# Performance work log

Hardware: AMD Instinct MI355X
Metric: run time of the kernel (lower is better)

Reference implementation:

```python
import jax, jax.numpy as jnp
import numpy as np

# Dimensions (match init_kwargs / input_specs)
NF, NLOC, NALL = 1, 1024, 2048
N_DIM, E_DIM, A_DIM = 128, 16, 64
NNEI, A_SEL, AXIS = 120, 20, 4

act = jax.nn.silu


def _lin(key, i, o):
    k1, k2 = jax.random.split(key)
    w = jax.random.normal(k1, (i, o), jnp.float32) / np.float32(np.sqrt(i))
    b = jax.random.normal(k2, (o,), jnp.float32) * 0.01
    return w, b


def setup_inputs() -> dict:
    key = jax.random.key(0)
    ks = jax.random.split(key, 16)
    d = {}
    d["node_ebd_ext"] = jax.random.normal(ks[0], (NF, NALL, N_DIM), jnp.float32)
    d["edge_ebd"] = jax.random.normal(ks[1], (NF, NLOC, NNEI, E_DIM), jnp.float32)
    d["h2"] = jax.random.normal(ks[2], (NF, NLOC, NNEI, 3), jnp.float32)
    d["angle_ebd"] = jax.random.normal(ks[3], (NF, NLOC, A_SEL, A_SEL, A_DIM), jnp.float32)
    d["sw"] = jax.random.uniform(ks[4], (NF, NLOC, NNEI), jnp.float32)
    d["a_sw"] = jax.random.uniform(ks[5], (NF, NLOC, A_SEL), jnp.float32)
    d["nlist"] = jax.random.randint(ks[6], (NF, NLOC, NNEI), 0, NALL)
    d["nlist_mask"] = jnp.ones((NF, NLOC, NNEI), bool)
    d["a_nlist_mask"] = jnp.ones((NF, NLOC, A_SEL), bool)
    edge_info_dim = 2 * N_DIM + E_DIM          # 272
    angle_dim = A_DIM + N_DIM + 2 * E_DIM      # 224 (a_compress_rate == 0)
    d["w_node_self"], d["b_node_self"] = _lin(ks[7], N_DIM, N_DIM)
    d["w_node_sym"], d["b_node_sym"] = _lin(ks[8], (N_DIM + E_DIM) * AXIS, N_DIM)
    d["w_node_edge"], d["b_node_edge"] = _lin(ks[9], edge_info_dim, N_DIM)
    d["w_edge_self"], d["b_edge_self"] = _lin(ks[10], edge_info_dim, E_DIM)
    d["w_ea1"], d["b_ea1"] = _lin(ks[11], angle_dim, E_DIM)
    d["w_ea2"], d["b_ea2"] = _lin(ks[12], E_DIM, E_DIM)
    d["w_angle_self"], d["b_angle_self"] = _lin(ks[13], angle_dim, A_DIM)
    # res_residual update style: one learnable residual scale per update branch,
    # init 'const' with update_residual = 0.1
    d["n_res"] = jnp.full((3, N_DIM), 0.1, jnp.float32)  # self, sym, edge-message
    d["e_res"] = jnp.full((2, E_DIM), 0.1, jnp.float32)  # self, angle-message
    d["a_res"] = jnp.full((1, A_DIM), 0.1, jnp.float32)  # self
    return d


def _forward(node_ebd_ext, edge_ebd, h2, angle_ebd, sw, a_sw,
             w_node_self, b_node_self, w_node_sym, b_node_sym,
             w_node_edge, b_node_edge, w_edge_self, b_edge_self,
             w_ea1, b_ea1, w_ea2, b_ea2, w_angle_self, b_angle_self,
             n_res, e_res, a_res, nlist, nlist_mask, a_nlist_mask):
    nf, nall, n_dim = node_ebd_ext.shape
    _, nloc, nnei, e_dim = edge_ebd.shape
    a_sel = angle_ebd.shape[2]
    node_ebd = node_ebd_ext[:, :nloc]

    # gather neighbor node embeddings: nf x nloc x nnei x n_dim
    nei_node = jax.vmap(lambda tbl, idx: tbl[idx])(node_ebd_ext, nlist)
    nei_node = jnp.where(nlist_mask[..., None], nei_node, 0.0)

    # 1) node self update
    node_self_update = act(node_ebd @ w_node_self + b_node_self)

    # 2) node symmetrization update (grrg over both edge and neighbor-node features)
    wgt = (sw * nlist_mask)[..., None]

    def sym(ebd):
        e = ebd * wgt
        hg = jnp.einsum('flni,flnd->flid', h2, e) / np.float32(nnei)  # f,l,3,d
        grrg = jnp.einsum('flid,flia->flda', hg, hg[..., :AXIS]) / np.float32(3.0)
        return grrg.reshape(nf, nloc, -1)

    node_sym_in = jnp.concatenate([sym(nei_node), sym(edge_ebd)], axis=-1)
    node_sym_update = act(node_sym_in @ w_node_sym + b_node_sym)

    # 3) edge info = [node_i, node_j, edge_ij]
    node_i = jnp.broadcast_to(node_ebd[:, :, None, :], (nf, nloc, nnei, n_dim))
    edge_info = jnp.concatenate([node_i, nei_node, edge_ebd], axis=-1)

    # 3a) node <- edge message (sw-weighted mean over neighbors)
    node_edge_update = act(edge_info @ w_node_edge + b_node_edge) * sw[..., None]
    node_edge_update = node_edge_update.sum(axis=-2) / np.float32(nnei)

    node_new = (node_ebd + n_res[0] * node_self_update
                + n_res[1] * node_sym_update + n_res[2] * node_edge_update)

    # 4) edge self update
    edge_self_update = act(edge_info @ w_edge_self + b_edge_self)

    # 5) angle branch (a_compress_rate == 0)
    edge_for_angle = jnp.where(a_nlist_mask[..., None], edge_ebd[:, :, :a_sel, :], 0.0)
    node_angle = jnp.broadcast_to(node_ebd[:, :, None, None, :], (nf, nloc, a_sel, a_sel, n_dim))
    e_ik = jnp.broadcast_to(edge_for_angle[:, :, :, None, :], (nf, nloc, a_sel, a_sel, e_dim))
    e_ij = jnp.broadcast_to(edge_for_angle[:, :, None, :, :], (nf, nloc, a_sel, a_sel, e_dim))
    angle_info = jnp.concatenate([angle_ebd, node_angle, e_ik, e_ij], axis=-1)

    # edge <- angle message: sw-weighted reduce over one angle axis
    ea = act(angle_info @ w_ea1 + b_ea1)  # nf,nloc,a_sel,a_sel,e_dim
    weighted = a_sw[:, :, :, None, None] * a_sw[:, :, None, :, None] * ea
    reduced = weighted.sum(axis=-2) / np.float32(np.sqrt(a_sel))  # nf,nloc,a_sel,e_dim
    pad = jnp.zeros((nf, nloc, nnei - a_sel, e_dim), edge_ebd.dtype)
    padded = jnp.concatenate([reduced, pad], axis=2)
    full_mask = jnp.concatenate(
        [a_nlist_mask, jnp.zeros((nf, nloc, nnei - a_sel), bool)], axis=-1)
    # smooth_edge_update = False: keep original edge ebd where angle mask is off
    padded = jnp.where(full_mask[..., None], padded, edge_ebd)
    edge_angle_update = act(padded @ w_ea2 + b_ea2)

    edge_new = edge_ebd + e_res[0] * edge_self_update + e_res[1] * edge_angle_update

    # angle self update
    angle_self_update = act(angle_info @ w_angle_self + b_angle_self)
    angle_new = angle_ebd + a_res[0] * angle_self_update

    return node_new, edge_new, angle_new


def reference(node_ebd_ext, edge_ebd, h2, angle_ebd, sw, a_sw, nlist, nlist_mask,
              a_nlist_mask, w_node_self, b_node_self, w_node_sym, b_node_sym,
              w_node_edge, b_node_edge, w_edge_self, b_edge_self, w_ea1, b_ea1,
              w_ea2, b_ea2, w_angle_self, b_angle_self, n_res, e_res, a_res):
    return _forward(node_ebd_ext, edge_ebd, h2, angle_ebd, sw, a_sw,
                    w_node_self, b_node_self, w_node_sym, b_node_sym,
                    w_node_edge, b_node_edge, w_edge_self, b_edge_self,
                    w_ea1, b_ea1, w_ea2, b_ea2, w_angle_self, b_angle_self,
                    n_res, e_res, a_res, nlist, nlist_mask, a_nlist_mask)
```

## Files before the change

### kernel.cpp

```cpp
#include <hip/hip_runtime.h>
#include <math.h>

#define NLOC 1024
#define NALL 2048
#define NDIM 128
#define EDIM 16
#define ADIM 64
#define NNEI 120
#define ASEL 20


__device__ __forceinline__ float silu(float x) {
    return x * __builtin_amdgcn_rcpf(1.f + __expf(-x));
}

__device__ __forceinline__ unsigned short f2bf(float f) {
    unsigned int u = __float_as_uint(f);
    u += 0x7fffu + ((u >> 16) & 1u);
    return (unsigned short)(u >> 16);
}

typedef __attribute__((ext_vector_type(8))) short bf16x8;
typedef __attribute__((ext_vector_type(4))) float f32x4;

__global__ __launch_bounds__(256) void k_prep(
    const float* __restrict__ node_ext,
    const float* __restrict__ w_ne, const float* __restrict__ b_ne,
    const float* __restrict__ w_es, const float* __restrict__ b_es,
    const float* __restrict__ w_ea1, const float* __restrict__ b_ea1,
    const float* __restrict__ w_as, const float* __restrict__ b_as,
    float* __restrict__ proj, float* __restrict__ pre_e,
    float* __restrict__ pre_a, unsigned short* __restrict__ wtb)
{
    const int b = blockIdx.x, t = threadIdx.x;
    if (b == 3072) {
        for (int idx = t; idx < 64 * 80; idx += 256) {
            int k = idx / 80, o = idx - k * 80;
            float v = (o < 16) ? w_ea1[k * 16 + o] : w_as[k * 64 + (o - 16)];
            wtb[o * 64 + k] = f2bf(v);
        }
        return;
    }
    __shared__ float x[128];
    const int row = (b < 2048) ? b : (b - 2048);
    if (t < 128) x[t] = node_ext[row * 128 + t];
    __syncthreads();
    if (b < 2048) {
        if (t < 144) {
            float acc = 0.f;
            if (t < 128) {
                for (int k = 0; k < 128; k++) acc += x[k] * w_ne[(128 + k) * 128 + t];
            } else {
                int o = t - 128;
                for (int k = 0; k < 128; k++) acc += x[k] * w_es[(128 + k) * 16 + o];
            }
            proj[b * 144 + t] = acc;
        }
    } else {
        int i = b - 2048;
        if (t < 144) {
            float acc;
            if (t < 128) {
                acc = b_ne[t];
                for (int k = 0; k < 128; k++) acc += x[k] * w_ne[k * 128 + t];
            } else {
                int o = t - 128;
                acc = b_es[o];
                for (int k = 0; k < 128; k++) acc += x[k] * w_es[k * 16 + o];
            }
            pre_e[i * 144 + t] = acc;
        } else if (t < 224) {
            int o = t - 144;
            float acc;
            if (o < 16) {
                acc = b_ea1[o];
                for (int k = 0; k < 128; k++) acc += x[k] * w_ea1[(64 + k) * 16 + o];
            } else {
                int o2 = o - 16;
                acc = b_as[o2];
                for (int k = 0; k < 128; k++) acc += x[k] * w_as[(64 + k) * 64 + o2];
            }
            pre_a[i * 80 + o] = acc;
        }
    }
}

__global__ __launch_bounds__(256, 4) void k_angle(
    const float* __restrict__ angle, const float* __restrict__ edge,
    const float* __restrict__ asw,
    const float* __restrict__ w_ea1, const float* __restrict__ w_as,
    const unsigned short* __restrict__ wtb, const float* __restrict__ pre_a,
    const float* __restrict__ a_res,
    float* __restrict__ out_angle, float* __restrict__ reduced)
{
    const int i = blockIdx.x, t = threadIdx.x;
    const int lane = t & 63, wv = t >> 6;
    const int m = lane & 15, q = lane >> 4;

    __shared__ float eca_s[ASEL * 80], ecb_s[ASEL * 80], edge20_s[ASEL * EDIM];
    __shared__ float asw_s[ASEL], ares_s[ADIM], red_s[ASEL * 16];

    bf16x8 bfrag[5][2];
    #pragma unroll
    for (int nt = 0; nt < 5; nt++)
        #pragma unroll
        for (int ks = 0; ks < 2; ks++)
            bfrag[nt][ks] = *(const bf16x8*)&wtb[(nt * 16 + m) * 64 + ks * 32 + q * 8];

    for (int idx = t; idx < ASEL * EDIM; idx += 256)
        edge20_s[idx] = edge[(size_t)i * NNEI * EDIM + idx];
    if (t < ASEL) asw_s[t] = asw[i * ASEL + t];
    if (t < ADIM) ares_s[t] = a_res[t];
    for (int idx = t; idx < ASEL * 16; idx += 256) red_s[idx] = 0.f;
    __syncthreads();

    int mt = wv;
    float4 c0, c1, c2, c3;
    {
        const float* Arow = angle + ((size_t)i * 400 + mt * 16 + m) * 64 + q * 8;
        c0 = *(const float4*)(Arow + 0);
        c1 = *(const float4*)(Arow + 4);
        c2 = *(const float4*)(Arow + 32);
        c3 = *(const float4*)(Arow + 36);
    }

    for (int idx = t; idx < 2 * ASEL * 80; idx += 256) {
        int half = idx / 1600, rem = idx - half * 1600;
        int aa = rem / 80, o = rem - aa * 80;
        float acc = (half == 0) ? pre_a[i * 80 + o] : 0.f;
        if (o < 16) {
            const float* w = w_ea1 + (192 + half * 16) * 16 + o;
            #pragma unroll
            for (int k = 0; k < 16; k++) acc += edge20_s[aa * 16 + k] * w[k * 16];
        } else {
            const float* w = w_as + (192 + half * 16) * 64 + (o - 16);
            #pragma unroll
            for (int k = 0; k < 16; k++) acc += edge20_s[aa * 16 + k] * w[k * 64];
        }
        if (half == 0) eca_s[rem] = acc; else ecb_s[rem] = acc;
    }
    __syncthreads();

    for (; mt < 25; mt += 4) {
        const int nmt = mt + 4;
        float4 n0{}, n1{}, n2{}, n3{};
        if (nmt < 25) {
            const float* Arow = angle + ((size_t)i * 400 + nmt * 16 + m) * 64 + q * 8;
            n0 = *(const float4*)(Arow + 0);
            n1 = *(const float4*)(Arow + 4);
            n2 = *(const float4*)(Arow + 32);
            n3 = *(const float4*)(Arow + 36);
        }

        bf16x8 af0, af1;
        af0[0] = (short)f2bf(c0.x); af0[1] = (short)f2bf(c0.y);
        af0[2] = (short)f2bf(c0.z); af0[3] = (short)f2bf(c0.w);
        af0[4] = (short)f2bf(c1.x); af0[5] = (short)f2bf(c1.y);
        af0[6] = (short)f2bf(c1.z); af0[7] = (short)f2bf(c1.w);
        af1[0] = (short)f2bf(c2.x); af1[1] = (short)f2bf(c2.y);
        af1[2] = (short)f2bf(c2.z); af1[3] = (short)f2bf(c2.w);
        af1[4] = (short)f2bf(c3.x); af1[5] = (short)f2bf(c3.y);
        af1[6] = (short)f2bf(c3.z); af1[7] = (short)f2bf(c3.w);

        const int p0 = mt * 16 + q * 4;
        float rez[4][4];
        #pragma unroll
        for (int r = 0; r < 4; r++) {
            const float* ar = angle + ((size_t)i * 400 + p0 + r) * 64 + m - 16;
            #pragma unroll
            for (int nt = 1; nt < 5; nt++) rez[r][nt - 1] = ar[nt * 16];
        }

        f32x4 acc[5];
        #pragma unroll
        for (int nt = 0; nt < 5; nt++) {
            acc[nt] = (f32x4){0.f, 0.f, 0.f, 0.f};
            acc[nt] = __builtin_amdgcn_mfma_f32_16x16x32_bf16(af0, bfrag[nt][0], acc[nt], 0, 0, 0);
            acc[nt] = __builtin_amdgcn_mfma_f32_16x16x32_bf16(af1, bfrag[nt][1], acc[nt], 0, 0, 0);
        }

        #pragma unroll
        for (int r = 0; r < 4; r++) {
            const int p = p0 + r;
            const int a = p / 20;
            const int bb = p - a * 20;
            {
                const float s = acc[0][r] + eca_s[a * 80 + m] + ecb_s[bb * 80 + m];
                atomicAdd(&red_s[a * 16 + m], asw_s[bb] * silu(s));
            }
            const size_t base = ((size_t)i * 400 + p) * 64;
            #pragma unroll
            for (int nt = 1; nt < 5; nt++) {
                const int o = nt * 16 + m;
                const float s = acc[nt][r] + eca_s[a * 80 + o] + ecb_s[bb * 80 + o];
                out_angle[base + o - 16] = rez[r][nt - 1] + ares_s[o - 16] * silu(s);
            }
        }

        c0 = n0; c1 = n1; c2 = n2; c3 = n3;
    }
    __syncthreads();

    for (int idx = t; idx < ASEL * 16; idx += 256) {
        const int aa = idx >> 4;
        reduced[i * 320 + idx] = red_s[idx] * asw_s[aa] * 0.22360679774997896f;
    }
}

__global__ __launch_bounds__(256) void k_en(
    const float* __restrict__ edge, const float* __restrict__ h2,
    const float* __restrict__ sw, const int* __restrict__ nlist,
    const float* __restrict__ node_ext,
    const float* __restrict__ w_ne, const float* __restrict__ w_es,
    const float* __restrict__ w_ea2, const float* __restrict__ b_ea2,
    const float* __restrict__ e_res,
    const float* __restrict__ proj, const float* __restrict__ pre_e,
    const float* __restrict__ reduced,
    const float* __restrict__ w_ns, const float* __restrict__ b_ns,
    const float* __restrict__ w_sym, const float* __restrict__ b_sym,
    const float* __restrict__ n_res,
    float* __restrict__ out_edge, float* __restrict__ out_node)
{
    const int i = blockIdx.x, t = threadIdx.x;
    __shared__ float red_s[320], esu_s[120 * 17], pre_e_s[144];
    __shared__ float wea2_s[256], bea2_s[16], eres_s[32], sw_s[120];
    __shared__ float wes_s[256];
    __shared__ float edge_s[120 * 17];
    __shared__ float neu_part[2][128], neu_s[128];
    __shared__ int nl_s[120];
    __shared__ float node_s[128], hjc_s[120 * 4], hgN_s[3 * 128], hgE_s[3 * 16], sym_s[576];
    __shared__ float hgN_part[2][3][128];
    __shared__ float hgE_part[8][3][16];
    __shared__ float s2_part[128];

    for (int idx = t; idx < 320; idx += 256) red_s[idx] = reduced[i * 320 + idx];
    for (int idx = t; idx < 1920; idx += 256) {
        const int j = idx >> 4, k = idx & 15;
        edge_s[j * 17 + k] = edge[(size_t)i * 1920 + idx];
    }
    if (t < 144) pre_e_s[t] = pre_e[i * 144 + t];
    if (t < 128) node_s[t] = node_ext[i * 128 + t];
    if (t < 120) {
        nl_s[t] = nlist[i * 120 + t];
        const float s = sw[i * 120 + t];
        sw_s[t] = s;
        hjc_s[t * 4 + 0] = h2[((size_t)i * 120 + t) * 3 + 0] * s;
        hjc_s[t * 4 + 1] = h2[((size_t)i * 120 + t) * 3 + 1] * s;
        hjc_s[t * 4 + 2] = h2[((size_t)i * 120 + t) * 3 + 2] * s;
        hjc_s[t * 4 + 3] = 0.f;
    }
    if (t < 256) wea2_s[t] = w_ea2[t];
    if (t < 16) bea2_s[t] = b_ea2[t];
    if (t < 32) eres_s[t] = e_res[t];
    for (int idx = t; idx < 256; idx += 256) wes_s[idx] = w_es[256 * 16 + idx];
    __syncthreads();

    {
        const int o = t & 127, half = t >> 7;
        const int j0 = half * 60, j1 = j0 + 60;
        float w3c[16];
        #pragma unroll
        for (int k = 0; k < 16; k++) w3c[k] = w_ne[(256 + k) * 128 + o];
        const float pe = pre_e_s[o];
        float pj = proj[(size_t)nl_s[j0] * 144 + o];
        float acc = 0.f;
        for (int j = j0; j < j1; j++) {
            float pn = 0.f;
            if (j + 1 < j1) pn = proj[(size_t)nl_s[j + 1] * 144 + o];
            const float* er = &edge_s[j * 17];
            float s = pe + pj;
            #pragma unroll
            for (int k = 0; k < 16; k++) s += er[k] * w3c[k];
            acc += silu(s) * sw_s[j];
            pj = pn;
        }
        neu_part[half][o] = acc;
    }

    for (int idx = t; idx < 1920; idx += 256) {
        const int j = idx >> 4, oo = idx & 15;
        const int n = nl_s[j];
        float s = pre_e_s[128 + oo] + proj[(size_t)n * 144 + 128 + oo];
        #pragma unroll
        for (int k = 0; k < 16; k++) s += edge_s[j * 17 + k] * wes_s[k * 16 + oo];
        esu_s[j * 17 + oo] = silu(s);
    }
    __syncthreads();

    if (t < 128) neu_s[t] = (neu_part[0][t] + neu_part[1][t]) * (1.f / 120.f);

    {
        const int d = t & 127, half = t >> 7;
        const int j0 = half * 60, j1 = j0 + 60;
        float a0 = 0.f, a1 = 0.f, a2 = 0.f;
        float v = node_ext[(size_t)nl_s[j0] * 128 + d];
        for (int j = j0; j < j1; j++) {
            float vn = 0.f;
            if (j + 1 < j1) vn = node_ext[(size_t)nl_s[j + 1] * 128 + d];
            const float4 hc = *(const float4*)&hjc_s[j * 4];
            a0 += hc.x * v; a1 += hc.y * v; a2 += hc.z * v;
            v = vn;
        }
        hgN_part[half][0][d] = a0;
        hgN_part[half][1][d] = a1;
        hgN_part[half][2][d] = a2;
    }

    if (t < 128) {
        const int d = t & 15, ch = t >> 4;
        const int j0 = ch * 15;
        float a0 = 0.f, a1 = 0.f, a2 = 0.f;
        for (int j = j0; j < j0 + 15; j++) {
            const float v = edge_s[j * 17 + d];
            const float4 hc = *(const float4*)&hjc_s[j * 4];
            a0 += hc.x * v; a1 += hc.y * v; a2 += hc.z * v;
        }
        hgE_part[ch][0][d] = a0;
        hgE_part[ch][1][d] = a1;
        hgE_part[ch][2][d] = a2;
    }

    for (int idx = t; idx < 1920; idx += 256) {
        const int j = idx >> 4, o = idx & 15;
        float s = bea2_s[o];
        if (j < 20) {
            #pragma unroll
            for (int k = 0; k < 16; k++) s += red_s[j * 16 + k] * wea2_s[k * 16 + o];
        } else {
            const float* er = &edge_s[j * 17];
            #pragma unroll
            for (int k = 0; k < 16; k++) s += er[k] * wea2_s[k * 16 + o];
        }
        const float eau = silu(s);
        const float ev = edge_s[j * 17 + o];
        out_edge[((size_t)i * 120 + j) * 16 + o] =
            ev + eres_s[o] * esu_s[j * 17 + o] + eres_s[16 + o] * eau;
    }
    __syncthreads();

    if (t < 128) {
        hgN_s[0 * 128 + t] = (hgN_part[0][0][t] + hgN_part[1][0][t]) * (1.f / 120.f);
        hgN_s[1 * 128 + t] = (hgN_part[0][1][t] + hgN_part[1][1][t]) * (1.f / 120.f);
        hgN_s[2 * 128 + t] = (hgN_part[0][2][t] + hgN_part[1][2][t]) * (1.f / 120.f);
    } else if (t < 176) {
        const int c = (t - 128) >> 4, d = (t - 128) & 15;
        float s = 0.f;
        #pragma unroll
        for (int ch = 0; ch < 8; ch++) s += hgE_part[ch][c][d];
        hgE_s[c * 16 + d] = s * (1.f / 120.f);
    }
    __syncthreads();

    for (int idx = t; idx < 576; idx += 256) {
        if (idx < 512) {
            const int d = idx >> 2, a = idx & 3;
            sym_s[idx] = (hgN_s[d] * hgN_s[a] + hgN_s[128 + d] * hgN_s[128 + a] +
                          hgN_s[256 + d] * hgN_s[256 + a]) * (1.f / 3.f);
        } else {
            const int r = idx - 512, d = r >> 2, a = r & 3;
            sym_s[idx] = (hgE_s[d] * hgE_s[a] + hgE_s[16 + d] * hgE_s[16 + a] +
                          hgE_s[32 + d] * hgE_s[32 + a]) * (1.f / 3.f);
        }
    }
    __syncthreads();

    float s1 = 0.f, s2 = 0.f;
    {
        const int o = t & 127, half = t >> 7;
        if (half == 0) {
            s1 = b_ns[o];
            for (int k = 0; k < 128; k++) s1 += node_s[k] * w_ns[k * 128 + o];
            s2 = b_sym[o];
            for (int k = 0; k < 224; k++) s2 += sym_s[k] * w_sym[k * 128 + o];
        } else {
            for (int k = 224; k < 576; k++) s2 += sym_s[k] * w_sym[k * 128 + o];
            s2_part[o] = s2;
        }
    }
    __syncthreads();

    if (t < 128) {
        const float nsu = silu(s1);
        const float nsy = silu(s2 + s2_part[t]);
        out_node[i * 128 + t] = node_s[t] + n_res[t] * nsu + n_res[128 + t] * nsy +
                                n_res[256 + t] * neu_s[t];
    }
}

extern "C" void kernel_launch(void* const* d_in, const int* in_sizes, int n_in,
                              void* d_out, int out_size, void* d_ws, size_t ws_size,
                              hipStream_t stream)
{
    const float* node_ext = (const float*)d_in[0];
    const float* edge     = (const float*)d_in[1];
    const float* h2       = (const float*)d_in[2];
    const float* angle    = (const float*)d_in[3];
    const float* sw       = (const float*)d_in[4];
    const float* asw      = (const float*)d_in[5];
    const int*   nlist    = (const int*)d_in[6];
    const float* w_ns  = (const float*)d_in[9];  const float* b_ns  = (const float*)d_in[10];
    const float* w_sym = (const float*)d_in[11]; const float* b_sym = (const float*)d_in[12];
    const float* w_ne  = (const float*)d_in[13]; const float* b_ne  = (const float*)d_in[14];
    const float* w_es  = (const float*)d_in[15]; const float* b_es  = (const float*)d_in[16];
    const float* w_ea1 = (const float*)d_in[17]; const float* b_ea1 = (const float*)d_in[18];
    const float* w_ea2 = (const float*)d_in[19]; const float* b_ea2 = (const float*)d_in[20];
    const float* w_as  = (const float*)d_in[21]; const float* b_as  = (const float*)d_in[22];
    const float* n_res = (const float*)d_in[23];
    const float* e_res = (const float*)d_in[24];
    const float* a_res = (const float*)d_in[25];

    float* out_node  = (float*)d_out;
    float* out_edge  = out_node + (size_t)NLOC * NDIM;
    float* out_angle = out_edge + (size_t)NLOC * NNEI * EDIM;

    float* ws      = (float*)d_ws;
    float* proj    = ws;
    float* pre_e   = proj + 2048 * 144;
    float* pre_a   = pre_e + 1024 * 144;
    float* reduced = pre_a + 1024 * 80;
    unsigned short* wtb = (unsigned short*)(reduced + 1024 * 320);

    k_prep<<<dim3(3073), dim3(256), 0, stream>>>(node_ext, w_ne, b_ne, w_es, b_es,
                                                 w_ea1, b_ea1, w_as, b_as,
                                                 proj, pre_e, pre_a, wtb);
    k_angle<<<dim3(1024), dim3(256), 0, stream>>>(angle, edge, asw, w_ea1, w_as,
                                                  wtb, pre_a, a_res, out_angle, reduced);
    k_en<<<dim3(1024), dim3(256), 0, stream>>>(edge, h2, sw, nlist, node_ext,
                                               w_ne, w_es, w_ea2, b_ea2, e_res,
                                               proj, pre_e, reduced,
                                               w_ns, b_ns, w_sym, b_sym, n_res,
                                               out_edge, out_node);
}
```

Baseline: 351.9 us.

## Fuse angle and edge/node kernels into one per-atom kernel with shared-memory union

```diff
diff --git a/kernel.cpp b/kernel.cpp
--- a/kernel.cpp
+++ b/kernel.cpp
@@ -85,20 +85,52 @@
     }
 }
 
-__global__ __launch_bounds__(256, 4) void k_angle(
+__global__ __launch_bounds__(256, 4) void k_fused(
     const float* __restrict__ angle, const float* __restrict__ edge,
     const float* __restrict__ asw,
     const float* __restrict__ w_ea1, const float* __restrict__ w_as,
     const unsigned short* __restrict__ wtb, const float* __restrict__ pre_a,
     const float* __restrict__ a_res,
-    float* __restrict__ out_angle, float* __restrict__ reduced)
+    const float* __restrict__ h2, const float* __restrict__ sw,
+    const int* __restrict__ nlist, const float* __restrict__ node_ext,
+    const float* __restrict__ w_ne, const float* __restrict__ w_es,
+    const float* __restrict__ w_ea2, const float* __restrict__ b_ea2,
+    const float* __restrict__ e_res,
+    const float* __restrict__ proj, const float* __restrict__ pre_e,
+    const float* __restrict__ w_ns, const float* __restrict__ b_ns,
+    const float* __restrict__ w_sym, const float* __restrict__ b_sym,
+    const float* __restrict__ n_res,
+    float* __restrict__ out_angle, float* __restrict__ out_edge,
+    float* __restrict__ out_node)
 {
     const int i = blockIdx.x, t = threadIdx.x;
     const int lane = t & 63, wv = t >> 6;
     const int m = lane & 15, q = lane >> 4;
 
-    __shared__ float eca_s[ASEL * 80], ecb_s[ASEL * 80], edge20_s[ASEL * EDIM];
-    __shared__ float asw_s[ASEL], ares_s[ADIM], red_s[ASEL * 16];
+    __shared__ float edge_s[120 * 17];
+    __shared__ float red_s[320];
+    __shared__ float asw_s[ASEL];
+
+    union SM {
+        struct {
+            float eca[ASEL * 80];
+            float ecb[ASEL * 80];
+            float ares[ADIM];
+        } a;
+        struct {
+            float esu[120 * 17];
+            float pre_e[144];
+            float wea2[256], bea2[16], eres[32], swv[120], wes[256];
+            float neu_part[2][128], neu[128];
+            float node[128], hjc[120 * 4];
+            float hgN[3 * 128], hgE[3 * 16], sym[576];
+            float hgN_part[2][3][128];
+            float hgE_part[8][3][16];
+            float s2_part[128];
+            int   nl[120];
+        } e;
+    };
+    __shared__ SM u;
 
     bf16x8 bfrag[5][2];
     #pragma unroll
@@ -107,11 +139,13 @@
         for (int ks = 0; ks < 2; ks++)
             bfrag[nt][ks] = *(const bf16x8*)&wtb[(nt * 16 + m) * 64 + ks * 32 + q * 8];
 
-    for (int idx = t; idx < ASEL * EDIM; idx += 256)
-        edge20_s[idx] = edge[(size_t)i * NNEI * EDIM + idx];
+    for (int idx = t; idx < 1920; idx += 256) {
+        const int j = idx >> 4, k = idx & 15;
+        edge_s[j * 17 + k] = edge[(size_t)i * 1920 + idx];
+    }
     if (t < ASEL) asw_s[t] = asw[i * ASEL + t];
-    if (t < ADIM) ares_s[t] = a_res[t];
-    for (int idx = t; idx < ASEL * 16; idx += 256) red_s[idx] = 0.f;
+    if (t < ADIM) u.a.ares[t] = a_res[t];
+    for (int idx = t; idx < 320; idx += 256) red_s[idx] = 0.f;
     __syncthreads();
 
     int mt = wv;
@@ -131,13 +165,13 @@
         if (o < 16) {
             const float* w = w_ea1 + (192 + half * 16) * 16 + o;
             #pragma unroll
-            for (int k = 0; k < 16; k++) acc += edge20_s[aa * 16 + k] * w[k * 16];
+            for (int k = 0; k < 16; k++) acc += edge_s[aa * 17 + k] * w[k * 16];
         } else {
             const float* w = w_as + (192 + half * 16) * 64 + (o - 16);
             #pragma unroll
-            for (int k = 0; k < 16; k++) acc += edge20_s[aa * 16 + k] * w[k * 64];
-        }
-        if (half == 0) eca_s[rem] = acc; else ecb_s[rem] = acc;
+            for (int k = 0; k < 16; k++) acc += edge_s[aa * 17 + k] * w[k * 64];
+        }
+        if (half == 0) u.a.eca[rem] = acc; else u.a.ecb[rem] = acc;
     }
     __syncthreads();
 
@@ -185,15 +219,15 @@
             const int a = p / 20;
             const int bb = p - a * 20;
             {
-                const float s = acc[0][r] + eca_s[a * 80 + m] + ecb_s[bb * 80 + m];
+                const float s = acc[0][r] + u.a.eca[a * 80 + m] + u.a.ecb[bb * 80 + m];
                 atomicAdd(&red_s[a * 16 + m], asw_s[bb] * silu(s));
             }
             const size_t base = ((size_t)i * 400 + p) * 64;
             #pragma unroll
             for (int nt = 1; nt < 5; nt++) {
                 const int o = nt * 16 + m;
-                const float s = acc[nt][r] + eca_s[a * 80 + o] + ecb_s[bb * 80 + o];
-                out_angle[base + o - 16] = rez[r][nt - 1] + ares_s[o - 16] * silu(s);
+                const float s = acc[nt][r] + u.a.eca[a * 80 + o] + u.a.ecb[bb * 80 + o];
+                out_angle[base + o - 16] = rez[r][nt - 1] + u.a.ares[o - 16] * silu(s);
             }
         }
 
@@ -201,58 +235,27 @@
     }
     __syncthreads();
 
-    for (int idx = t; idx < ASEL * 16; idx += 256) {
+    for (int idx = t; idx < 320; idx += 256) {
         const int aa = idx >> 4;
-        reduced[i * 320 + idx] = red_s[idx] * asw_s[aa] * 0.22360679774997896f;
-    }
-}
-
-__global__ __launch_bounds__(256) void k_en(
-    const float* __restrict__ edge, const float* __restrict__ h2,
-    const float* __restrict__ sw, const int* __restrict__ nlist,
-    const float* __restrict__ node_ext,
-    const float* __restrict__ w_ne, const float* __restrict__ w_es,
-    const float* __restrict__ w_ea2, const float* __restrict__ b_ea2,
-    const float* __restrict__ e_res,
-    const float* __restrict__ proj, const float* __restrict__ pre_e,
-    const float* __restrict__ reduced,
-    const float* __restrict__ w_ns, const float* __restrict__ b_ns,
-    const float* __restrict__ w_sym, const float* __restrict__ b_sym,
-    const float* __restrict__ n_res,
-    float* __restrict__ out_edge, float* __restrict__ out_node)
-{
-    const int i = blockIdx.x, t = threadIdx.x;
-    __shared__ float red_s[320], esu_s[120 * 17], pre_e_s[144];
-    __shared__ float wea2_s[256], bea2_s[16], eres_s[32], sw_s[120];
-    __shared__ float wes_s[256];
-    __shared__ float edge_s[120 * 17];
-    __shared__ float neu_part[2][128], neu_s[128];
-    __shared__ int nl_s[120];
-    __shared__ float node_s[128], hjc_s[120 * 4], hgN_s[3 * 128], hgE_s[3 * 16], sym_s[576];
-    __shared__ float hgN_part[2][3][128];
-    __shared__ float hgE_part[8][3][16];
-    __shared__ float s2_part[128];
-
-    for (int idx = t; idx < 320; idx += 256) red_s[idx] = reduced[i * 320 + idx];
-    for (int idx = t; idx < 1920; idx += 256) {
-        const int j = idx >> 4, k = idx & 15;
-        edge_s[j * 17 + k] = edge[(size_t)i * 1920 + idx];
-    }
-    if (t < 144) pre_e_s[t] = pre_e[i * 144 + t];
-    if (t < 128) node_s[t] = node_ext[i * 128 + t];
+        red_s[idx] *= asw_s[aa] * 0.22360679774997896f;
+    }
+    __syncthreads();
+
+    if (t < 144) u.e.pre_e[t] = pre_e[i * 144 + t];
+    if (t < 128) u.e.node[t] = node_ext[i * 128 + t];
     if (t < 120) {
-        nl_s[t] = nlist[i * 120 + t];
+        u.e.nl[t] = nlist[i * 120 + t];
         const float s = sw[i * 120 + t];
-        sw_s[t] = s;
-        hjc_s[t * 4 + 0] = h2[((size_t)i * 120 + t) * 3 + 0] * s;
-        hjc_s[t * 4 + 1] = h2[((size_t)i * 120 + t) * 3 + 1] * s;
-        hjc_s[t * 4 + 2] = h2[((size_t)i * 120 + t) * 3 + 2] * s;
-        hjc_s[t * 4 + 3] = 0.f;
-    }
-    if (t < 256) wea2_s[t] = w_ea2[t];
-    if (t < 16) bea2_s[t] = b_ea2[t];
-    if (t < 32) eres_s[t] = e_res[t];
-    for (int idx = t; idx < 256; idx += 256) wes_s[idx] = w_es[256 * 16 + idx];
+        u.e.swv[t] = s;
+        u.e.hjc[t * 4 + 0] = h2[((size_t)i * 120 + t) * 3 + 0] * s;
+        u.e.hjc[t * 4 + 1] = h2[((size_t)i * 120 + t) * 3 + 1] * s;
+        u.e.hjc[t * 4 + 2] = h2[((size_t)i * 120 + t) * 3 + 2] * s;
+        u.e.hjc[t * 4 + 3] = 0.f;
+    }
+    if (t < 256) u.e.wea2[t] = w_ea2[t];
+    if (t < 16) u.e.bea2[t] = b_ea2[t];
+    if (t < 32) u.e.eres[t] = e_res[t];
+    for (int idx = t; idx < 256; idx += 256) u.e.wes[idx] = w_es[256 * 16 + idx];
     __syncthreads();
 
     {
@@ -261,49 +264,61 @@
         float w3c[16];
         #pragma unroll
         for (int k = 0; k < 16; k++) w3c[k] = w_ne[(256 + k) * 128 + o];
-        const float pe = pre_e_s[o];
-        float pj = proj[(size_t)nl_s[j0] * 144 + o];
-        float acc = 0.f;
-        for (int j = j0; j < j1; j++) {
-            float pn = 0.f;
-            if (j + 1 < j1) pn = proj[(size_t)nl_s[j + 1] * 144 + o];
-            const float* er = &edge_s[j * 17];
-            float s = pe + pj;
-            #pragma unroll
-            for (int k = 0; k < 16; k++) s += er[k] * w3c[k];
-            acc += silu(s) * sw_s[j];
-            pj = pn;
-        }
-        neu_part[half][o] = acc;
+        const float pe = u.e.pre_e[o];
+        float pjA = proj[(size_t)u.e.nl[j0] * 144 + o];
+        float pjB = proj[(size_t)u.e.nl[j0 + 1] * 144 + o];
+        float accA = 0.f, accB = 0.f;
+        for (int j = j0; j < j1; j += 2) {
+            float pnA = 0.f, pnB = 0.f;
+            if (j + 2 < j1) {
+                pnA = proj[(size_t)u.e.nl[j + 2] * 144 + o];
+                pnB = proj[(size_t)u.e.nl[j + 3] * 144 + o];
+            }
+            const float* erA = &edge_s[j * 17];
+            const float* erB = &edge_s[(j + 1) * 17];
+            float sA = pe + pjA, sB = pe + pjB;
+            #pragma unroll
+            for (int k = 0; k < 16; k++) { sA += erA[k] * w3c[k]; sB += erB[k] * w3c[k]; }
+            accA += silu(sA) * u.e.swv[j];
+            accB += silu(sB) * u.e.swv[j + 1];
+            pjA = pnA; pjB = pnB;
+        }
+        u.e.neu_part[half][o] = accA + accB;
     }
 
     for (int idx = t; idx < 1920; idx += 256) {
         const int j = idx >> 4, oo = idx & 15;
-        const int n = nl_s[j];
-        float s = pre_e_s[128 + oo] + proj[(size_t)n * 144 + 128 + oo];
-        #pragma unroll
-        for (int k = 0; k < 16; k++) s += edge_s[j * 17 + k] * wes_s[k * 16 + oo];
-        esu_s[j * 17 + oo] = silu(s);
-    }
-    __syncthreads();
-
-    if (t < 128) neu_s[t] = (neu_part[0][t] + neu_part[1][t]) * (1.f / 120.f);
+        const int n = u.e.nl[j];
+        float s = u.e.pre_e[128 + oo] + proj[(size_t)n * 144 + 128 + oo];
+        #pragma unroll
+        for (int k = 0; k < 16; k++) s += edge_s[j * 17 + k] * u.e.wes[k * 16 + oo];
+        u.e.esu[j * 17 + oo] = silu(s);
+    }
+    __syncthreads();
+
+    if (t < 128) u.e.neu[t] = (u.e.neu_part[0][t] + u.e.neu_part[1][t]) * (1.f / 120.f);
 
     {
         const int d = t & 127, half = t >> 7;
         const int j0 = half * 60, j1 = j0 + 60;
-        float a0 = 0.f, a1 = 0.f, a2 = 0.f;
-        float v = node_ext[(size_t)nl_s[j0] * 128 + d];
-        for (int j = j0; j < j1; j++) {
-            float vn = 0.f;
-            if (j + 1 < j1) vn = node_ext[(size_t)nl_s[j + 1] * 128 + d];
-            const float4 hc = *(const float4*)&hjc_s[j * 4];
-            a0 += hc.x * v; a1 += hc.y * v; a2 += hc.z * v;
-            v = vn;
-        }
-        hgN_part[half][0][d] = a0;
-        hgN_part[half][1][d] = a1;
-        hgN_part[half][2][d] = a2;
+        float a0 = 0.f, a1 = 0.f, a2 = 0.f, b0 = 0.f, b1 = 0.f, b2 = 0.f;
+        float vA = node_ext[(size_t)u.e.nl[j0] * 128 + d];
+        float vB = node_ext[(size_t)u.e.nl[j0 + 1] * 128 + d];
+        for (int j = j0; j < j1; j += 2) {
+            float vnA = 0.f, vnB = 0.f;
+            if (j + 2 < j1) {
+                vnA = node_ext[(size_t)u.e.nl[j + 2] * 128 + d];
+                vnB = node_ext[(size_t)u.e.nl[j + 3] * 128 + d];
+            }
+            const float4 hA = *(const float4*)&u.e.hjc[j * 4];
+            const float4 hB = *(const float4*)&u.e.hjc[(j + 1) * 4];
+            a0 += hA.x * vA; a1 += hA.y * vA; a2 += hA.z * vA;
+            b0 += hB.x * vB; b1 += hB.y * vB; b2 += hB.z * vB;
+            vA = vnA; vB = vnB;
+        }
+        u.e.hgN_part[half][0][d] = a0 + b0;
+        u.e.hgN_part[half][1][d] = a1 + b1;
+        u.e.hgN_part[half][2][d] = a2 + b2;
     }
 
     if (t < 128) {
@@ -312,54 +327,54 @@
         float a0 = 0.f, a1 = 0.f, a2 = 0.f;
         for (int j = j0; j < j0 + 15; j++) {
             const float v = edge_s[j * 17 + d];
-            const float4 hc = *(const float4*)&hjc_s[j * 4];
+            const float4 hc = *(const float4*)&u.e.hjc[j * 4];
             a0 += hc.x * v; a1 += hc.y * v; a2 += hc.z * v;
         }
-        hgE_part[ch][0][d] = a0;
-        hgE_part[ch][1][d] = a1;
-        hgE_part[ch][2][d] = a2;
+        u.e.hgE_part[ch][0][d] = a0;
+        u.e.hgE_part[ch][1][d] = a1;
+        u.e.hgE_part[ch][2][d] = a2;
     }
 
     for (int idx = t; idx < 1920; idx += 256) {
         const int j = idx >> 4, o = idx & 15;
-        float s = bea2_s[o];
+        float s = u.e.bea2[o];
         if (j < 20) {
             #pragma unroll
-            for (int k = 0; k < 16; k++) s += red_s[j * 16 + k] * wea2_s[k * 16 + o];
+            for (int k = 0; k < 16; k++) s += red_s[j * 16 + k] * u.e.wea2[k * 16 + o];
         } else {
             const float* er = &edge_s[j * 17];
             #pragma unroll
-            for (int k = 0; k < 16; k++) s += er[k] * wea2_s[k * 16 + o];
+            for (int k = 0; k < 16; k++) s += er[k] * u.e.wea2[k * 16 + o];
         }
         const float eau = silu(s);
         const float ev = edge_s[j * 17 + o];
         out_edge[((size_t)i * 120 + j) * 16 + o] =
-            ev + eres_s[o] * esu_s[j * 17 + o] + eres_s[16 + o] * eau;
+            ev + u.e.eres[o] * u.e.esu[j * 17 + o] + u.e.eres[16 + o] * eau;
     }
     __syncthreads();
 
     if (t < 128) {
-        hgN_s[0 * 128 + t] = (hgN_part[0][0][t] + hgN_part[1][0][t]) * (1.f / 120.f);
-        hgN_s[1 * 128 + t] = (hgN_part[0][1][t] + hgN_part[1][1][t]) * (1.f / 120.f);
-        hgN_s[2 * 128 + t] = (hgN_part[0][2][t] + hgN_part[1][2][t]) * (1.f / 120.f);
+        u.e.hgN[0 * 128 + t] = (u.e.hgN_part[0][0][t] + u.e.hgN_part[1][0][t]) * (1.f / 120.f);
+        u.e.hgN[1 * 128 + t] = (u.e.hgN_part[0][1][t] + u.e.hgN_part[1][1][t]) * (1.f / 120.f);
+        u.e.hgN[2 * 128 + t] = (u.e.hgN_part[0][2][t] + u.e.hgN_part[1][2][t]) * (1.f / 120.f);
     } else if (t < 176) {
         const int c = (t - 128) >> 4, d = (t - 128) & 15;
         float s = 0.f;
         #pragma unroll
-        for (int ch = 0; ch < 8; ch++) s += hgE_part[ch][c][d];
-        hgE_s[c * 16 + d] = s * (1.f / 120.f);
+        for (int ch = 0; ch < 8; ch++) s += u.e.hgE_part[ch][c][d];
+        u.e.hgE[c * 16 + d] = s * (1.f / 120.f);
     }
     __syncthreads();
 
     for (int idx = t; idx < 576; idx += 256) {
         if (idx < 512) {
             const int d = idx >> 2, a = idx & 3;
-            sym_s[idx] = (hgN_s[d] * hgN_s[a] + hgN_s[128 + d] * hgN_s[128 + a] +
-                          hgN_s[256 + d] * hgN_s[256 + a]) * (1.f / 3.f);
+            u.e.sym[idx] = (u.e.hgN[d] * u.e.hgN[a] + u.e.hgN[128 + d] * u.e.hgN[128 + a] +
+                            u.e.hgN[256 + d] * u.e.hgN[256 + a]) * (1.f / 3.f);
         } else {
             const int r = idx - 512, d = r >> 2, a = r & 3;
-            sym_s[idx] = (hgE_s[d] * hgE_s[a] + hgE_s[16 + d] * hgE_s[16 + a] +
-                          hgE_s[32 + d] * hgE_s[32 + a]) * (1.f / 3.f);
+            u.e.sym[idx] = (u.e.hgE[d] * u.e.hgE[a] + u.e.hgE[16 + d] * u.e.hgE[16 + a] +
+                            u.e.hgE[32 + d] * u.e.hgE[32 + a]) * (1.f / 3.f);
         }
     }
     __syncthreads();
@@ -369,21 +384,21 @@
         const int o = t & 127, half = t >> 7;
         if (half == 0) {
             s1 = b_ns[o];
-            for (int k = 0; k < 128; k++) s1 += node_s[k] * w_ns[k * 128 + o];
+            for (int k = 0; k < 128; k++) s1 += u.e.node[k] * w_ns[k * 128 + o];
             s2 = b_sym[o];
-            for (int k = 0; k < 224; k++) s2 += sym_s[k] * w_sym[k * 128 + o];
+            for (int k = 0; k < 224; k++) s2 += u.e.sym[k] * w_sym[k * 128 + o];
         } else {
-            for (int k = 224; k < 576; k++) s2 += sym_s[k] * w_sym[k * 128 + o];
-            s2_part[o] = s2;
+            for (int k = 224; k < 576; k++) s2 += u.e.sym[k] * w_sym[k * 128 + o];
+            u.e.s2_part[o] = s2;
         }
     }
     __syncthreads();
 
     if (t < 128) {
         const float nsu = silu(s1);
-        const float nsy = silu(s2 + s2_part[t]);
-        out_node[i * 128 + t] = node_s[t] + n_res[t] * nsu + n_res[128 + t] * nsy +
-                                n_res[256 + t] * neu_s[t];
+        const float nsy = silu(s2 + u.e.s2_part[t]);
+        out_node[i * 128 + t] = u.e.node[t] + n_res[t] * nsu + n_res[128 + t] * nsy +
+                                n_res[256 + t] * u.e.neu[t];
     }
 }
 
@@ -417,17 +432,16 @@
     float* proj    = ws;
     float* pre_e   = proj + 2048 * 144;
     float* pre_a   = pre_e + 1024 * 144;
-    float* reduced = pre_a + 1024 * 80;
-    unsigned short* wtb = (unsigned short*)(reduced + 1024 * 320);
+    unsigned short* wtb = (unsigned short*)(pre_a + 1024 * 80);
 
     k_prep<<<dim3(3073), dim3(256), 0, stream>>>(node_ext, w_ne, b_ne, w_es, b_es,
                                                  w_ea1, b_ea1, w_as, b_as,
                                                  proj, pre_e, pre_a, wtb);
-    k_angle<<<dim3(1024), dim3(256), 0, stream>>>(angle, edge, asw, w_ea1, w_as,
-                                                  wtb, pre_a, a_res, out_angle, reduced);
-    k_en<<<dim3(1024), dim3(256), 0, stream>>>(edge, h2, sw, nlist, node_ext,
-                                               w_ne, w_es, w_ea2, b_ea2, e_res,
-                                               proj, pre_e, reduced,
-                                               w_ns, b_ns, w_sym, b_sym, n_res,
-                                               out_edge, out_node);
+    k_fused<<<dim3(1024), dim3(256), 0, stream>>>(angle, edge, asw, w_ea1, w_as,
+                                                  wtb, pre_a, a_res,
+                                                  h2, sw, nlist, node_ext,
+                                                  w_ne, w_es, w_ea2, b_ea2, e_res,
+                                                  proj, pre_e,
+                                                  w_ns, b_ns, w_sym, b_sym, n_res,
+                                                  out_angle, out_edge, out_node);
 }
```

After: 336.0 us. 1.05x faster.
